# Kernel optimization log

Hardware: AMD Instinct MI355X
Metric: run time of the kernel (lower is better)

## Reference

```python
import jax, jax.numpy as jnp
import numpy as np
import math

B, T, C = 1, 2048, 512
NH, NKV, HD, W = 8, 4, 64, 128  # heads, kv heads, head_dim, window_size
THETA = 10000.0
EPS = 1e-6


def _rms(x, w):
    # RMSNorm over last (head_dim) axis with learnable scale w
    return x * jax.lax.rsqrt(jnp.mean(x * x, axis=-1, keepdims=True) + EPS) * w


def _rope(x, cos, sin):
    # x: (B, H, T, HD); cos/sin: (T, HD//2). Half-split rotation.
    h = x.shape[-1] // 2
    x1, x2 = x[..., :h], x[..., h:]
    return jnp.concatenate([x1 * cos - x2 * sin, x2 * cos + x1 * sin], axis=-1)


def setup_inputs():
    key = jax.random.key(0)
    ks = jax.random.split(key, 5)
    x = jax.random.normal(ks[0], (B, T, C), jnp.float32)
    s = 1.0 / math.sqrt(C)
    W_q = jax.random.normal(ks[1], (C, NH * HD), jnp.float32) * s
    W_k = jax.random.normal(ks[2], (C, NKV * HD), jnp.float32) * s
    W_v = jax.random.normal(ks[3], (C, NKV * HD), jnp.float32) * s
    W_o = jax.random.normal(ks[4], (C, C), jnp.float32) * s
    q_norm_w = jnp.ones((HD,), jnp.float32)
    k_norm_w = jnp.ones((HD,), jnp.float32)
    pos = jnp.arange(T, dtype=jnp.float32)
    inv_freq = 1.0 / (THETA ** (jnp.arange(0, HD, 2, dtype=jnp.float32) / HD))
    ang = pos[:, None] * inv_freq[None, :]  # (T, HD//2)
    return {"x": x, "W_q": W_q, "W_k": W_k, "W_v": W_v, "W_o": W_o,
            "q_norm_w": q_norm_w, "k_norm_w": k_norm_w,
            "cos": jnp.cos(ang), "sin": jnp.sin(ang)}


def reference(x, W_q, W_k, W_v, W_o, q_norm_w, k_norm_w, cos, sin):
    q = (x @ W_q).reshape(B, T, NH, HD).transpose(0, 2, 1, 3)   # (B,NH,T,HD)
    k = (x @ W_k).reshape(B, T, NKV, HD).transpose(0, 2, 1, 3)  # (B,NKV,T,HD)
    v = (x @ W_v).reshape(B, T, NKV, HD).transpose(0, 2, 1, 3)
    q = _rope(q, cos, sin)
    k = _rope(k, cos, sin)
    q = _rms(q, q_norm_w)
    k = _rms(k, k_norm_w)
    g = NH // NKV  # GQA group size
    k = jnp.repeat(k, g, axis=1)  # (B,NH,T,HD)
    v = jnp.repeat(v, g, axis=1)
    # causal sliding-window: gather W-length windows ending at each position
    kp = jnp.pad(k, ((0, 0), (0, 0), (W - 1, 0), (0, 0)))
    vp = jnp.pad(v, ((0, 0), (0, 0), (W - 1, 0), (0, 0)))
    idx = jnp.arange(T)[:, None] + jnp.arange(W)[None, :]  # (T, W)
    kw = kp[:, :, idx, :]  # (B,NH,T,W,HD)
    vw = vp[:, :, idx, :]
    valid = jnp.arange(W)[None, :] >= (W - 1 - jnp.arange(T))[:, None]  # (T,W)
    attn = jnp.einsum('bhtd,bhtwd->bhtw', q, kw) / math.sqrt(HD)
    attn = jnp.where(valid[None, None], attn, -jnp.inf)
    attn = jax.nn.softmax(attn, axis=-1)
    out = jnp.einsum('bhtw,bhtwd->bhtd', attn, vw)  # (B,NH,T,HD)
    out = out.transpose(0, 2, 1, 3).reshape(B, T, C)
    return out @ W_o
```

## Files before the change

kernel.cpp:

```cpp
#include <hip/hip_runtime.h>
#include <hip/hip_bf16.h>
#include <math.h>

typedef float  f32x4  __attribute__((ext_vector_type(4)));
typedef short  s16x4  __attribute__((ext_vector_type(4)));
typedef short  s16x8  __attribute__((ext_vector_type(8)));
typedef unsigned short u16;

__device__ inline u16 f2b(float f) {
    __hip_bfloat16 h = __float2bfloat16(f);
    return *reinterpret_cast<u16*>(&h);
}
__device__ inline float b2f(u16 v) {
    return __uint_as_float(((unsigned)v) << 16);
}
__device__ inline void st_out(float* p, float v) { *p = v; }
__device__ inline void st_out(u16* p, float v)   { *p = f2b(v); }

__global__ __launch_bounds__(256) void prep(const float* __restrict__ x,
    const float* __restrict__ Wq, const float* __restrict__ Wk,
    const float* __restrict__ Wv, const float* __restrict__ Wo,
    u16* __restrict__ xb, u16* __restrict__ Wt, u16* __restrict__ Wot)
{
    const int tid = threadIdx.x, bid = blockIdx.x;
    if (bid >= 192) {
        int i = ((bid - 192) * 256 + tid) * 8;
        float4 v0 = *(const float4*)(x + i);
        float4 v1 = *(const float4*)(x + i + 4);
        ushort4 o0 = { f2b(v0.x), f2b(v0.y), f2b(v0.z), f2b(v0.w) };
        ushort4 o1 = { f2b(v1.x), f2b(v1.y), f2b(v1.z), f2b(v1.w) };
        *(ushort4*)(xb + i)     = o0;
        *(ushort4*)(xb + i + 4) = o1;
        return;
    }
    __shared__ u16 Tsh[64][72];
    const float* src; u16* dst; int N, base, kt, nt;
    if (bid < 64)       { src = Wq; dst = Wt;  N = 512; base = 0;   kt = bid >> 3;       nt = bid & 7; }
    else if (bid < 96)  { src = Wk; dst = Wt;  N = 256; base = 512; kt = (bid-64) >> 2;  nt = (bid-64) & 3; }
    else if (bid < 128) { src = Wv; dst = Wt;  N = 256; base = 768; kt = (bid-96) >> 2;  nt = (bid-96) & 3; }
    else                { src = Wo; dst = Wot; N = 512; base = 0;   kt = (bid-128) >> 3; nt = (bid-128) & 7; }
    const int k0 = kt * 64, n0 = nt * 64;
    const int r = tid >> 2, c0 = (tid & 3) * 16;
#pragma unroll
    for (int j = 0; j < 4; ++j) {
        float4 v = *(const float4*)(src + (size_t)(k0 + r) * N + n0 + c0 + j * 4);
        Tsh[c0 + j*4 + 0][r] = f2b(v.x);
        Tsh[c0 + j*4 + 1][r] = f2b(v.y);
        Tsh[c0 + j*4 + 2][r] = f2b(v.z);
        Tsh[c0 + j*4 + 3][r] = f2b(v.w);
    }
    __syncthreads();
    const int n = tid >> 2, kc = (tid & 3) * 16;
    u16* op = dst + (size_t)(base + n0 + n) * 512 + k0 + kc;
    *(s16x8*)(op)     = *(const s16x8*)&Tsh[n][kc];
    *(s16x8*)(op + 8) = *(const s16x8*)&Tsh[n][kc + 8];
}

template<typename OutT>
__global__ __launch_bounds__(256) void gemm_mfma(const u16* __restrict__ A,
    const u16* __restrict__ Bt, OutT* __restrict__ C, int ldc)
{
    __shared__ u16 Ash[64][72];
    __shared__ u16 Bsh[64][72];
    const int tid = threadIdx.x;
    const int m0b = blockIdx.y * 64, n0b = blockIdx.x * 64;
    const int lane = tid & 63, wv = tid >> 6;
    const int q = lane & 15, g = lane >> 4;
    const int wm = (wv & 1) * 32, wn = (wv >> 1) * 32;
    const int sr = tid >> 2, sc = (tid & 3) * 16;
    f32x4 acc[2][2] = {{{0,0,0,0},{0,0,0,0}},{{0,0,0,0},{0,0,0,0}}};
    for (int k0 = 0; k0 < 512; k0 += 64) {
        s16x8 a0 = *(const s16x8*)(A  + (size_t)(m0b + sr) * 512 + k0 + sc);
        s16x8 a1 = *(const s16x8*)(A  + (size_t)(m0b + sr) * 512 + k0 + sc + 8);
        s16x8 b0 = *(const s16x8*)(Bt + (size_t)(n0b + sr) * 512 + k0 + sc);
        s16x8 b1 = *(const s16x8*)(Bt + (size_t)(n0b + sr) * 512 + k0 + sc + 8);
        __syncthreads();
        *(s16x8*)&Ash[sr][sc]     = a0;
        *(s16x8*)&Ash[sr][sc + 8] = a1;
        *(s16x8*)&Bsh[sr][sc]     = b0;
        *(s16x8*)&Bsh[sr][sc + 8] = b1;
        __syncthreads();
#pragma unroll
        for (int kk = 0; kk < 64; kk += 32) {
            s16x8 af0 = *(const s16x8*)&Ash[wm + q][kk + g*8];
            s16x8 af1 = *(const s16x8*)&Ash[wm + 16 + q][kk + g*8];
            s16x8 bf0 = *(const s16x8*)&Bsh[wn + q][kk + g*8];
            s16x8 bf1 = *(const s16x8*)&Bsh[wn + 16 + q][kk + g*8];
            acc[0][0] = __builtin_amdgcn_mfma_f32_16x16x32_bf16(af0, bf0, acc[0][0], 0, 0, 0);
            acc[0][1] = __builtin_amdgcn_mfma_f32_16x16x32_bf16(af0, bf1, acc[0][1], 0, 0, 0);
            acc[1][0] = __builtin_amdgcn_mfma_f32_16x16x32_bf16(af1, bf0, acc[1][0], 0, 0, 0);
            acc[1][1] = __builtin_amdgcn_mfma_f32_16x16x32_bf16(af1, bf1, acc[1][1], 0, 0, 0);
        }
    }
#pragma unroll
    for (int mt = 0; mt < 2; ++mt)
#pragma unroll
        for (int nt = 0; nt < 2; ++nt)
#pragma unroll
            for (int r = 0; r < 4; ++r)
                st_out(&C[(size_t)(m0b + wm + mt*16 + g*4 + r) * ldc + n0b + wn + nt*16 + q],
                       acc[mt][nt][r]);
}

__global__ __launch_bounds__(256) void swa_mfma(const u16* __restrict__ qkvb,
    const float* __restrict__ cosT, const float* __restrict__ sinT,
    const float* __restrict__ qw, const float* __restrict__ kw,
    u16* __restrict__ attb)
{
    __shared__ u16 Ksh[160][72];
    __shared__ u16 Vt[64][162];
    const int tid = threadIdx.x;
    const int kvh = blockIdx.y;
    const int t0 = blockIdx.x * 32;
    for (int i = 0; i < 5; ++i) {
        int idx = i * 256 + tid;
        int j = idx >> 3, e = idx & 7, d0 = e * 8;
        int kt = t0 - 127 + j;
        if (kt < 0 || kt >= 2048) {
            s16x8 z = {0,0,0,0,0,0,0,0};
            *(s16x8*)&Ksh[j][d0] = z;
        } else {
            s16x8 raw = *(const s16x8*)(qkvb + (size_t)kt * 1024 + 512 + kvh * 64 + d0);
            float kv[8], ov[8];
#pragma unroll
            for (int ii = 0; ii < 8; ++ii) kv[ii] = b2f((u16)raw[ii]);
#pragma unroll
            for (int ii = 0; ii < 8; ++ii) ov[ii] = __shfl_xor(kv[ii], 4);
            const float* cp = cosT + kt * 32 + (e & 3) * 8;
            const float* sp = sinT + kt * 32 + (e & 3) * 8;
            float4 c0 = *(const float4*)(cp), c1 = *(const float4*)(cp + 4);
            float4 s0 = *(const float4*)(sp), s1 = *(const float4*)(sp + 4);
            float cf[8] = {c0.x,c0.y,c0.z,c0.w,c1.x,c1.y,c1.z,c1.w};
            float sf[8] = {s0.x,s0.y,s0.z,s0.w,s1.x,s1.y,s1.z,s1.w};
            const bool lo = (e < 4);
            float r[8]; float ssl = 0.f;
#pragma unroll
            for (int ii = 0; ii < 8; ++ii) {
                r[ii] = lo ? (kv[ii]*cf[ii] - ov[ii]*sf[ii])
                           : (kv[ii]*cf[ii] + ov[ii]*sf[ii]);
                ssl += r[ii] * r[ii];
            }
            ssl += __shfl_xor(ssl, 1);
            ssl += __shfl_xor(ssl, 2);
            ssl += __shfl_xor(ssl, 4);
            float scale = rsqrtf(ssl * (1.0f / 64.0f) + 1e-6f);
            float4 w0 = *(const float4*)(kw + d0), w1 = *(const float4*)(kw + d0 + 4);
            float wf[8] = {w0.x,w0.y,w0.z,w0.w,w1.x,w1.y,w1.z,w1.w};
            s16x8 outv;
#pragma unroll
            for (int ii = 0; ii < 8; ++ii) outv[ii] = (short)f2b(r[ii] * scale * wf[ii]);
            *(s16x8*)&Ksh[j][d0] = outv;
        }
    }
    for (int cch = 0; cch < 5; ++cch) {
        int w  = cch * 32 + (tid & 31);
        int d0 = (tid >> 5) * 8;
        int kt = t0 - 127 + w;
        s16x8 val = {0,0,0,0,0,0,0,0};
        if (kt >= 0 && kt < 2048)
            val = *(const s16x8*)(qkvb + (size_t)kt * 1024 + 768 + kvh * 64 + d0);
#pragma unroll
        for (int jj = 0; jj < 8; ++jj) Vt[d0 + jj][w] = ((const u16*)&val)[jj];
    }
    const int wv = tid >> 6, lane = tid & 63;
    const int q = lane & 15, g = lane >> 4;
    const int h  = 2 * kvh + (wv >> 1);
    const int tw = t0 + (wv & 1) * 16;
    const int jb = (wv & 1) * 16;
    const int t = tw + q;
    s16x8 qf0, qf1;
    {
        const u16* qp = qkvb + (size_t)t * 1024 + h * 64;
        s16x8 q0r = *(const s16x8*)(qp + g * 8);
        s16x8 q1r = *(const s16x8*)(qp + 32 + g * 8);
        const float* cp = cosT + t * 32 + g * 8;
        const float* sp = sinT + t * 32 + g * 8;
        float4 c0 = *(const float4*)(cp), c1 = *(const float4*)(cp + 4);
        float4 s0 = *(const float4*)(sp), s1 = *(const float4*)(sp + 4);
        float cf[8] = {c0.x,c0.y,c0.z,c0.w,c1.x,c1.y,c1.z,c1.w};
        float sf[8] = {s0.x,s0.y,s0.z,s0.w,s1.x,s1.y,s1.z,s1.w};
        float rl[8], rh[8]; float ssl = 0.f;
#pragma unroll
        for (int ii = 0; ii < 8; ++ii) {
            float ql = b2f((u16)q0r[ii]), qh = b2f((u16)q1r[ii]);
            rl[ii] = ql * cf[ii] - qh * sf[ii];
            rh[ii] = qh * cf[ii] + ql * sf[ii];
            ssl += rl[ii]*rl[ii] + rh[ii]*rh[ii];
        }
        ssl += __shfl_xor(ssl, 16);
        ssl += __shfl_xor(ssl, 32);
        float scale = rsqrtf(ssl * (1.0f / 64.0f) + 1e-6f);
        float4 wl0 = *(const float4*)(qw + g * 8), wl1 = *(const float4*)(qw + g * 8 + 4);
        float4 wh0 = *(const float4*)(qw + 32 + g * 8), wh1 = *(const float4*)(qw + 32 + g * 8 + 4);
        float wlo[8] = {wl0.x,wl0.y,wl0.z,wl0.w,wl1.x,wl1.y,wl1.z,wl1.w};
        float whi[8] = {wh0.x,wh0.y,wh0.z,wh0.w,wh1.x,wh1.y,wh1.z,wh1.w};
#pragma unroll
        for (int ii = 0; ii < 8; ++ii) {
            qf0[ii] = (short)f2b(rl[ii] * scale * wlo[ii]);
            qf1[ii] = (short)f2b(rh[ii] * scale * whi[ii]);
        }
    }
    __syncthreads();
    float s[9][4];
    float mx = -INFINITY;
    for (int wt = 0; wt < 9; ++wt) {
        int ldsrow = jb + wt * 16 + q;
        s16x8 kf0 = *(const s16x8*)&Ksh[ldsrow][g * 8];
        s16x8 kf1 = *(const s16x8*)&Ksh[ldsrow][32 + g * 8];
        f32x4 accv = {0, 0, 0, 0};
        accv = __builtin_amdgcn_mfma_f32_16x16x32_bf16(kf0, qf0, accv, 0, 0, 0);
        accv = __builtin_amdgcn_mfma_f32_16x16x32_bf16(kf1, qf1, accv, 0, 0, 0);
#pragma unroll
        for (int r = 0; r < 4; ++r) {
            int woff = wt * 16 + g * 4 + r;
            int key  = tw - 127 + woff;
            bool ok = (woff >= q) && (woff <= q + 127) && (key >= 0);
            float sv = ok ? accv[r] * 0.125f : -INFINITY;
            s[wt][r] = sv;
            mx = fmaxf(mx, sv);
        }
    }
    mx = fmaxf(mx, __shfl_xor(mx, 16));
    mx = fmaxf(mx, __shfl_xor(mx, 32));
    float sum = 0.f;
    s16x4 pb[9];
    for (int wt = 0; wt < 9; ++wt) {
#pragma unroll
        for (int r = 0; r < 4; ++r) {
            float p = __expf(s[wt][r] - mx);
            sum += p;
            pb[wt][r] = (short)f2b(p);
        }
    }
    sum += __shfl_xor(sum, 16);
    sum += __shfl_xor(sum, 32);
    float inv = 1.0f / sum;
    f32x4 oacc[4];
#pragma unroll
    for (int dt = 0; dt < 4; ++dt) {
        f32x4 a = {0, 0, 0, 0};
        for (int wt = 0; wt < 9; ++wt) {
            int col = jb + wt * 16 + g * 4;
            s16x4 vf = *(const s16x4*)&Vt[dt * 16 + q][col];
            a = __builtin_amdgcn_mfma_f32_16x16x16bf16_1k(vf, pb[wt], a, 0, 0, 0);
        }
        oacc[dt] = a;
    }
    __syncthreads();
    float (*Osh)[16][68] = (float (*)[16][68])&Ksh[0][0];
#pragma unroll
    for (int dt = 0; dt < 4; ++dt)
#pragma unroll
        for (int r = 0; r < 4; ++r)
            Osh[wv][q][dt * 16 + g * 4 + r] = oacc[dt][r] * inv;
    __syncthreads();
    const int qq = lane >> 2, dd0 = (lane & 3) * 16;
    u16* op = attb + (size_t)(tw + qq) * 512 + h * 64 + dd0;
#pragma unroll
    for (int jj = 0; jj < 4; ++jj) {
        float4 vvv = *(const float4*)&Osh[wv][qq][dd0 + jj * 4];
        ushort4 ov = { f2b(vvv.x), f2b(vvv.y), f2b(vvv.z), f2b(vvv.w) };
        *(ushort4*)(op + jj * 4) = ov;
    }
}

extern "C" void kernel_launch(void* const* d_in, const int* in_sizes, int n_in,
                              void* d_out, int out_size, void* d_ws, size_t ws_size,
                              hipStream_t stream)
{
    const float* x    = (const float*)d_in[0];
    const float* Wq   = (const float*)d_in[1];
    const float* Wk   = (const float*)d_in[2];
    const float* Wv   = (const float*)d_in[3];
    const float* Wo   = (const float*)d_in[4];
    const float* qw   = (const float*)d_in[5];
    const float* kw   = (const float*)d_in[6];
    const float* cosT = (const float*)d_in[7];
    const float* sinT = (const float*)d_in[8];

    u16* ws   = (u16*)d_ws;
    u16* xb   = ws;
    u16* Wt   = xb   + (size_t)2048 * 512;
    u16* Wot  = Wt   + (size_t)1024 * 512;
    u16* qkvb = Wot  + (size_t)512 * 512;
    u16* attb = qkvb + (size_t)2048 * 1024;

    dim3 blk(256);
    hipLaunchKernelGGL(prep, dim3(704), blk, 0, stream, x, Wq, Wk, Wv, Wo, xb, Wt, Wot);
    hipLaunchKernelGGL((gemm_mfma<u16>), dim3(16, 32), blk, 0, stream, xb, Wt, qkvb, 1024);
    hipLaunchKernelGGL(swa_mfma, dim3(64, 4), blk, 0, stream,
                       qkvb, cosT, sinT, qw, kw, attb);
    hipLaunchKernelGGL((gemm_mfma<float>), dim3(8, 32), blk, 0, stream,
                       attb, Wot, (float*)d_out, 512);
}
```

Measured before the change: 34.33 us.

## Use direct global-to-LDS loads in GEMM with XOR-swizzled pre-permuted operands

The GEMM tile loads now go straight from global memory into LDS via global_load_lds, skipping the register staging and the separate LDS store. Because that path can't pad rows, the producers (prep's x conversion, weight transposes and the attention output) now write their bf16 buffers with an XOR chunk swizzle inside each 64-element block. The GEMM fragment reads use the matching swizzle to avoid bank conflicts. The risk is a layout mismatch: every producer and consumer must agree on the permutation, and the load still sits behind barriers with no double buffering.

```diff
diff --git a/kernel.cpp b/kernel.cpp
--- a/kernel.cpp
+++ b/kernel.cpp
@@ -16,6 +16,12 @@
 }
 __device__ inline void st_out(float* p, float v) { *p = v; }
 __device__ inline void st_out(u16* p, float v)   { *p = f2b(v); }
+
+__device__ inline void gload16(const void* g, void* l) {
+    __builtin_amdgcn_global_load_lds(
+        (const __attribute__((address_space(1))) void*)g,
+        (__attribute__((address_space(3))) void*)l, 16, 0, 0);
+}
 
 __global__ __launch_bounds__(256) void prep(const float* __restrict__ x,
     const float* __restrict__ Wq, const float* __restrict__ Wk,
@@ -25,12 +31,16 @@
     const int tid = threadIdx.x, bid = blockIdx.x;
     if (bid >= 192) {
         int i = ((bid - 192) * 256 + tid) * 8;
+        int row = i >> 9, col = i & 511;
+        int scol = (col & ~63) | ((((col >> 3) & 7) ^ (row & 7)) << 3);
         float4 v0 = *(const float4*)(x + i);
         float4 v1 = *(const float4*)(x + i + 4);
-        ushort4 o0 = { f2b(v0.x), f2b(v0.y), f2b(v0.z), f2b(v0.w) };
-        ushort4 o1 = { f2b(v1.x), f2b(v1.y), f2b(v1.z), f2b(v1.w) };
-        *(ushort4*)(xb + i)     = o0;
-        *(ushort4*)(xb + i + 4) = o1;
+        s16x8 o;
+        o[0] = (short)f2b(v0.x); o[1] = (short)f2b(v0.y);
+        o[2] = (short)f2b(v0.z); o[3] = (short)f2b(v0.w);
+        o[4] = (short)f2b(v1.x); o[5] = (short)f2b(v1.y);
+        o[6] = (short)f2b(v1.z); o[7] = (short)f2b(v1.w);
+        *(s16x8*)(xb + (size_t)row * 512 + scol) = o;
         return;
     }
     __shared__ u16 Tsh[64][72];
@@ -51,41 +61,46 @@
     }
     __syncthreads();
     const int n = tid >> 2, kc = (tid & 3) * 16;
-    u16* op = dst + (size_t)(base + n0 + n) * 512 + k0 + kc;
-    *(s16x8*)(op)     = *(const s16x8*)&Tsh[n][kc];
-    *(s16x8*)(op + 8) = *(const s16x8*)&Tsh[n][kc + 8];
+    const int r7 = n & 7;
+    const int cc0 = (kc >> 3) ^ r7;
+    const int cc1 = ((kc >> 3) + 1) ^ r7;
+    u16* oprow = dst + (size_t)(base + n0 + n) * 512 + k0;
+    *(s16x8*)(oprow + cc0 * 8) = *(const s16x8*)&Tsh[n][kc];
+    *(s16x8*)(oprow + cc1 * 8) = *(const s16x8*)&Tsh[n][kc + 8];
 }
 
 template<typename OutT>
 __global__ __launch_bounds__(256) void gemm_mfma(const u16* __restrict__ A,
     const u16* __restrict__ Bt, OutT* __restrict__ C, int ldc)
 {
-    __shared__ u16 Ash[64][72];
-    __shared__ u16 Bsh[64][72];
+    __shared__ u16 Ash[64][64];
+    __shared__ u16 Bsh[64][64];
     const int tid = threadIdx.x;
     const int m0b = blockIdx.y * 64, n0b = blockIdx.x * 64;
     const int lane = tid & 63, wv = tid >> 6;
     const int q = lane & 15, g = lane >> 4;
     const int wm = (wv & 1) * 32, wn = (wv >> 1) * 32;
-    const int sr = tid >> 2, sc = (tid & 3) * 16;
+    const int lrow = lane >> 3, lchunk = lane & 7;
+    const int s7 = q & 7;
     f32x4 acc[2][2] = {{{0,0,0,0},{0,0,0,0}},{{0,0,0,0},{0,0,0,0}}};
     for (int k0 = 0; k0 < 512; k0 += 64) {
-        s16x8 a0 = *(const s16x8*)(A  + (size_t)(m0b + sr) * 512 + k0 + sc);
-        s16x8 a1 = *(const s16x8*)(A  + (size_t)(m0b + sr) * 512 + k0 + sc + 8);
-        s16x8 b0 = *(const s16x8*)(Bt + (size_t)(n0b + sr) * 512 + k0 + sc);
-        s16x8 b1 = *(const s16x8*)(Bt + (size_t)(n0b + sr) * 512 + k0 + sc + 8);
         __syncthreads();
-        *(s16x8*)&Ash[sr][sc]     = a0;
-        *(s16x8*)&Ash[sr][sc + 8] = a1;
-        *(s16x8*)&Bsh[sr][sc]     = b0;
-        *(s16x8*)&Bsh[sr][sc + 8] = b1;
+#pragma unroll
+        for (int is = 0; is < 2; ++is) {
+            const int rbase = is * 32 + wv * 8;
+            gload16(A  + (size_t)(m0b + rbase + lrow) * 512 + k0 + lchunk * 8,
+                    &Ash[rbase][0]);
+            gload16(Bt + (size_t)(n0b + rbase + lrow) * 512 + k0 + lchunk * 8,
+                    &Bsh[rbase][0]);
+        }
         __syncthreads();
 #pragma unroll
         for (int kk = 0; kk < 64; kk += 32) {
-            s16x8 af0 = *(const s16x8*)&Ash[wm + q][kk + g*8];
-            s16x8 af1 = *(const s16x8*)&Ash[wm + 16 + q][kk + g*8];
-            s16x8 bf0 = *(const s16x8*)&Bsh[wn + q][kk + g*8];
-            s16x8 bf1 = *(const s16x8*)&Bsh[wn + 16 + q][kk + g*8];
+            const int cs = ((kk >> 3) + g) ^ s7;
+            s16x8 af0 = *(const s16x8*)&Ash[wm + q][cs * 8];
+            s16x8 af1 = *(const s16x8*)&Ash[wm + 16 + q][cs * 8];
+            s16x8 bf0 = *(const s16x8*)&Bsh[wn + q][cs * 8];
+            s16x8 bf1 = *(const s16x8*)&Bsh[wn + 16 + q][cs * 8];
             acc[0][0] = __builtin_amdgcn_mfma_f32_16x16x32_bf16(af0, bf0, acc[0][0], 0, 0, 0);
             acc[0][1] = __builtin_amdgcn_mfma_f32_16x16x32_bf16(af0, bf1, acc[0][1], 0, 0, 0);
             acc[1][0] = __builtin_amdgcn_mfma_f32_16x16x32_bf16(af1, bf0, acc[1][0], 0, 0, 0);
@@ -255,13 +270,17 @@
             Osh[wv][q][dt * 16 + g * 4 + r] = oacc[dt][r] * inv;
     __syncthreads();
     const int qq = lane >> 2, dd0 = (lane & 3) * 16;
-    u16* op = attb + (size_t)(tw + qq) * 512 + h * 64 + dd0;
-#pragma unroll
-    for (int jj = 0; jj < 4; ++jj) {
-        float4 vvv = *(const float4*)&Osh[wv][qq][dd0 + jj * 4];
-        ushort4 ov = { f2b(vvv.x), f2b(vvv.y), f2b(vvv.z), f2b(vvv.w) };
-        *(ushort4*)(op + jj * 4) = ov;
-    }
+    const int r7 = qq & 7;
+    u16* oprow = attb + (size_t)(tw + qq) * 512 + h * 64;
+    s16x8 v0, v1;
+#pragma unroll
+    for (int j = 0; j < 8; ++j) v0[j] = (short)f2b(Osh[wv][qq][dd0 + j]);
+#pragma unroll
+    for (int j = 0; j < 8; ++j) v1[j] = (short)f2b(Osh[wv][qq][dd0 + 8 + j]);
+    const int cc0 = (dd0 >> 3) ^ r7;
+    const int cc1 = ((dd0 >> 3) + 1) ^ r7;
+    *(s16x8*)(oprow + cc0 * 8) = v0;
+    *(s16x8*)(oprow + cc1 * 8) = v1;
 }
 
 extern "C" void kernel_launch(void* const* d_in, const int* in_sizes, int n_in,
```

Measured after the change: 34.19 us. About the same (-0.4%).
